# Kernel optimization log

Measured on AMD Instinct MI355X. Metric: run time of the kernel, lower is better.

## Reference

```python
import jax, jax.numpy as jnp
import numpy as np

B, T = 256, 1024
V, E, H = 27, 64, 128


def setup_inputs() -> dict:
    key = jax.random.key(0)
    ks = jax.random.split(key, 8)
    return {
        "x": jax.random.randint(ks[0], (B, T), 0, V, dtype=jnp.int32),
        "emb": jax.random.normal(ks[1], (V, E), dtype=jnp.float32) * 0.02,
        "wx0": jax.random.normal(ks[2], (E, 4 * H), dtype=jnp.float32) * 0.01,
        "wh0": jax.random.normal(ks[3], (H, 4 * H), dtype=jnp.float32) * 0.01,
        "b0": jnp.zeros((4 * H,), dtype=jnp.float32),
        "wx1": jax.random.normal(ks[4], (H, 4 * H), dtype=jnp.float32) * 0.01,
        "wh1": jax.random.normal(ks[5], (H, 4 * H), dtype=jnp.float32) * 0.01,
        "b1": jnp.zeros((4 * H,), dtype=jnp.float32),
        "why": jax.random.normal(ks[6], (H, V), dtype=jnp.float32),
        "by": jnp.zeros((V,), dtype=jnp.float32),
    }


def _cell(xt, h_prev, c_prev, wx, wh, b):
    # gates: [B, 4H]; chunk order matches torch .chunk(4): f, i, g, o
    gates = xt @ wx + h_prev @ wh + b
    ft, it, gt, ot = jnp.split(gates, 4, axis=1)
    c_t = jax.nn.sigmoid(ft) * c_prev + jax.nn.sigmoid(it) * jnp.tanh(gt)
    h_t = jnp.tanh(c_t) * jax.nn.sigmoid(ot)
    return h_t, c_t


def reference(x, emb, wx0, wh0, b0, wx1, wh1, b1, why, by):
    Bx = x.shape[0]
    xe = emb[x]                       # [B, T, E]
    xe = jnp.swapaxes(xe, 0, 1)       # [T, B, E] for scan over time
    h0 = jnp.zeros((Bx, H), jnp.float32)
    c0 = jnp.zeros((Bx, H), jnp.float32)
    h1 = jnp.zeros((Bx, H), jnp.float32)
    c1 = jnp.zeros((Bx, H), jnp.float32)

    def step(carry, xt):
        h0, c0, h1, c1 = carry
        h0, c0 = _cell(xt, h0, c0, wx0, wh0, b0)   # layer 0
        h1, c1 = _cell(h0, h1, c1, wx1, wh1, b1)   # layer 1 (dropout off in eval)
        yt = h1 @ why + by                         # [B, V]
        return (h0, c0, h1, c1), yt

    _, ys = jax.lax.scan(step, (h0, c0, h1, c1), xe)  # ys: [T, B, V]
    return jnp.swapaxes(ys, 0, 1)                     # [B, T, V]
```

## Files before the change

kernel.cpp:

```cpp
#include <hip/hip_runtime.h>


#define B_  256
#define T_  1024
#define V_  27
#define E_  64
#define H_  128
#define G4  512
#define TPITCH 528

template <int CTRL>
__device__ __forceinline__ float dppmov(float v) {
    return __int_as_float(__builtin_amdgcn_update_dpp(
               0, __float_as_int(v), CTRL, 0xF, 0xF, true));
}
__device__ __forceinline__ float sum8(float v) {
    v += dppmov<0xB1>(v);
    v += dppmov<0x4E>(v);
    v += dppmov<0x141>(v);
    return v;
}
__device__ __forceinline__ float tanh_fast(float y) {
    const float t = __expf(2.f * y);
    return fmaf(-2.f, __builtin_amdgcn_rcpf(t + 1.f), 1.f);
}

#define REPEAT16(M) M(0) M(1) M(2) M(3) M(4) M(5) M(6) M(7) \
                    M(8) M(9) M(10) M(11) M(12) M(13) M(14) M(15)

#define DECLW(K) float wf##K, wi##K, wg##K, wo##K;
#define LOADW(K) wf##K = wrow[(size_t)(K)*G4 + p]; \
                 wi##K = wrow[(size_t)(K)*G4 + H_ + p]; \
                 wg##K = wrow[(size_t)(K)*G4 + 2*H_ + p]; \
                 wo##K = wrow[(size_t)(K)*G4 + 3*H_ + p];
#define FMAK(K, HV, C) sf = fmaf(HV.C, wf##K, sf); \
                       si = fmaf(HV.C, wi##K, si); \
                       sg_ = fmaf(HV.C, wg##K, sg_); \
                       so = fmaf(HV.C, wo##K, so);

__global__ __launch_bounds__(G4)
void build_table0(const float* __restrict__ emb,
                  const float* __restrict__ wx0,
                  const float* __restrict__ b0,
                  float* __restrict__ table0)
{
    const int v = blockIdx.x;
    const int j = threadIdx.x;
    __shared__ float e[E_];
    if (j < E_) e[j] = emb[v * E_ + j];
    __syncthreads();
    float s = b0[j];
#pragma unroll 8
    for (int k = 0; k < E_; ++k) s += e[k] * wx0[k * G4 + j];
    const int r = j & (H_ - 1), gate = j >> 7;
    table0[v * TPITCH + gate * 132 + r] = s;
}

__global__ __launch_bounds__(1024, 4)
void lstm_l0_chunk(const int* __restrict__ x,
                   const float* __restrict__ table0,
                   const float* __restrict__ wh0,
                   float* __restrict__ h0st, float* __restrict__ c0st,
                   float* __restrict__ h0buf,
                   int t0, int TC)
{
    const int j = threadIdx.x;
    const int p = j >> 3;
    const int e = j & 7;
    const int b = blockIdx.x;
    const int gate = e & 3;

    __shared__ __align__(16) float hP[2][8][20];

    const float* wrow = wh0 + (size_t)(16 * e) * G4;
    REPEAT16(DECLW)
    REPEAT16(LOADW)
    if (j < H_) hP[0][j >> 4][j & 15] = h0st[b * H_ + j];
    float c = c0st[b * H_ + p];
    float hh = 0.f;
    __syncthreads();

    const int* xb = x + (size_t)b * T_ + t0;
    float* hob = h0buf + (size_t)b * TC * H_;
    const float A = (gate == 2) ? 2.f : 1.f;
    const int toff = gate * 132 + p;
    const bool e0 = (e & 1), e1 = (e & 2);

    float tv = table0[xb[0] * TPITCH + toff];
    for (int t = 0; t < TC; ++t) {
        const int idxn = (t + 1 < TC) ? xb[t + 1] : 0;

        const float4* hb4 = reinterpret_cast<const float4*>(&hP[t & 1][e][0]);
        const float4 h0v = hb4[0], h1v = hb4[1], h2v = hb4[2], h3v = hb4[3];

        float sf = 0.f, si = 0.f, sg_ = 0.f, so = 0.f;
        FMAK(0,  h0v, x) FMAK(1,  h0v, y) FMAK(2,  h0v, z) FMAK(3,  h0v, w)
        FMAK(4,  h1v, x) FMAK(5,  h1v, y) FMAK(6,  h1v, z) FMAK(7,  h1v, w)
        FMAK(8,  h2v, x) FMAK(9,  h2v, y) FMAK(10, h2v, z) FMAK(11, h2v, w)
        FMAK(12, h3v, x) FMAK(13, h3v, y) FMAK(14, h3v, z) FMAK(15, h3v, w)

        const float rf = sum8(sf);
        const float ri = sum8(si);
        const float rg = sum8(sg_);
        const float ro = sum8(so);

        const float s0 = e0 ? ri : rf;
        const float s1 = e0 ? ro : rg;
        const float val = (e1 ? s1 : s0) + tv;

        const float tz  = __expf(A * val);
        const float act = fmaf(-A, __builtin_amdgcn_rcpf(tz + 1.f), 1.f);

        const float iv = dppmov<0x39>(act);
        const float gv = dppmov<0x4E>(act);
        const float ov = dppmov<0x93>(act);
        c  = fmaf(act, c, iv * gv);
        hh = tanh_fast(c) * ov;

        if (e == 0) {
            hP[(t + 1) & 1][p >> 4][p & 15] = hh;
            hob[(size_t)t * H_ + p] = hh;
        }
        tv = table0[idxn * TPITCH + toff];
        __syncthreads();
    }
    if (e == 0) { h0st[b * H_ + p] = hh; c0st[b * H_ + p] = c; }
}

__global__ __launch_bounds__(G4, 2)
void gemm_xg1(const float* __restrict__ h0buf,
              const float* __restrict__ wx1,
              const float* __restrict__ b1,
              float* __restrict__ xg1)
{
    const int j  = threadIdx.x;
    const size_t m0 = (size_t)blockIdx.x * 64;
    const int c  = j & 127;
    const int rg = j >> 7;

    __shared__ __align__(16) float aT[64 * 132];

#pragma unroll
    for (int i = 0; i < 4; ++i) {
        const int e  = i * G4 + j;
        const int r  = e >> 5;
        const int k4 = e & 31;
        const float4 v = *reinterpret_cast<const float4*>(&h0buf[(m0 + r) * H_ + k4 * 4]);
        *reinterpret_cast<float4*>(&aT[r * 132 + k4 * 4]) = v;
    }
    __syncthreads();

    float acc[4][16];
#pragma unroll
    for (int cc = 0; cc < 4; ++cc)
#pragma unroll
        for (int rr = 0; rr < 16; ++rr) acc[cc][rr] = 0.f;

    for (int k4 = 0; k4 < 32; ++k4) {
        float bv[4][4];
#pragma unroll
        for (int kk = 0; kk < 4; ++kk)
#pragma unroll
            for (int cc = 0; cc < 4; ++cc)
                bv[kk][cc] = wx1[(size_t)(k4 * 4 + kk) * G4 + cc * 128 + c];
#pragma unroll
        for (int rr = 0; rr < 16; ++rr) {
            const float4 av = *reinterpret_cast<const float4*>(&aT[(rg * 16 + rr) * 132 + k4 * 4]);
#pragma unroll
            for (int cc = 0; cc < 4; ++cc) {
                acc[cc][rr] = fmaf(av.x, bv[0][cc], acc[cc][rr]);
                acc[cc][rr] = fmaf(av.y, bv[1][cc], acc[cc][rr]);
                acc[cc][rr] = fmaf(av.z, bv[2][cc], acc[cc][rr]);
                acc[cc][rr] = fmaf(av.w, bv[3][cc], acc[cc][rr]);
            }
        }
    }

    float b1v[4];
#pragma unroll
    for (int cc = 0; cc < 4; ++cc) b1v[cc] = b1[cc * 128 + c];
#pragma unroll
    for (int rr = 0; rr < 16; ++rr) {
        const size_t row = m0 + rg * 16 + rr;
#pragma unroll
        for (int cc = 0; cc < 4; ++cc)
            xg1[row * G4 + cc * 128 + c] = acc[cc][rr] + b1v[cc];
    }
}

__global__ __launch_bounds__(1024, 4)
void lstm_l1_chunk(const float* __restrict__ xg1,
                   const float* __restrict__ wh1,
                   float* __restrict__ h1st, float* __restrict__ c1st,
                   float* __restrict__ h1buf,
                   int TC)
{
    const int j = threadIdx.x;
    const int p = j >> 3;
    const int e = j & 7;
    const int b = blockIdx.x;
    const int gate = e & 3;

    __shared__ __align__(16) float hP[2][8][20];

    const float* wrow = wh1 + (size_t)(16 * e) * G4;
    REPEAT16(DECLW)
    REPEAT16(LOADW)
    if (j < H_) hP[0][j >> 4][j & 15] = h1st[b * H_ + j];
    float c = c1st[b * H_ + p];
    float hh = 0.f;
    __syncthreads();

    const float* xgb = xg1 + (size_t)b * TC * G4;
    float* hob = h1buf + (size_t)b * TC * H_;
    const float A = (gate == 2) ? 2.f : 1.f;
    const int xcol = gate * H_ + p;
    const bool e0 = (e & 1), e1 = (e & 2);

    float xv = xgb[xcol];
    for (int t = 0; t < TC; ++t) {
        const float xvn = (t + 1 < TC) ? xgb[(size_t)(t + 1) * G4 + xcol] : 0.f;

        const float4* hb4 = reinterpret_cast<const float4*>(&hP[t & 1][e][0]);
        const float4 h0v = hb4[0], h1v = hb4[1], h2v = hb4[2], h3v = hb4[3];

        float sf = 0.f, si = 0.f, sg_ = 0.f, so = 0.f;
        FMAK(0,  h0v, x) FMAK(1,  h0v, y) FMAK(2,  h0v, z) FMAK(3,  h0v, w)
        FMAK(4,  h1v, x) FMAK(5,  h1v, y) FMAK(6,  h1v, z) FMAK(7,  h1v, w)
        FMAK(8,  h2v, x) FMAK(9,  h2v, y) FMAK(10, h2v, z) FMAK(11, h2v, w)
        FMAK(12, h3v, x) FMAK(13, h3v, y) FMAK(14, h3v, z) FMAK(15, h3v, w)

        const float rf = sum8(sf);
        const float ri = sum8(si);
        const float rg = sum8(sg_);
        const float ro = sum8(so);

        const float s0 = e0 ? ri : rf;
        const float s1 = e0 ? ro : rg;
        const float val = (e1 ? s1 : s0) + xv;

        const float tz  = __expf(A * val);
        const float act = fmaf(-A, __builtin_amdgcn_rcpf(tz + 1.f), 1.f);

        const float iv = dppmov<0x39>(act);
        const float gv = dppmov<0x4E>(act);
        const float ov = dppmov<0x93>(act);
        c  = fmaf(act, c, iv * gv);
        hh = tanh_fast(c) * ov;

        if (e == 0) {
            hP[(t + 1) & 1][p >> 4][p & 15] = hh;
            hob[(size_t)t * H_ + p] = hh;
        }
        xv = xvn;
        __syncthreads();
    }
    if (e == 0) { h1st[b * H_ + p] = hh; c1st[b * H_ + p] = c; }
}

__global__ __launch_bounds__(256)
void proj_y(const float* __restrict__ h1buf,
            const float* __restrict__ why,
            const float* __restrict__ by,
            float* __restrict__ out,
            int t0, int TC)
{
    const int tid = threadIdx.x;
    const int b   = blockIdx.x;

    __shared__ __align__(16) float whyS[V_][H_];
    __shared__ float byS[V_];
    __shared__ float yS[256][29];

    for (int e = tid; e < V_ * H_; e += 256) {
        const int v = e / H_, k = e - v * H_;
        whyS[v][k] = why[k * V_ + v];
    }
    if (tid < V_) byS[tid] = by[tid];
    __syncthreads();

    const float* hb  = h1buf + (size_t)b * TC * H_;
    float* outb      = out + ((size_t)b * T_ + t0) * V_;

    for (int tt0 = 0; tt0 < TC; tt0 += 256) {
        const int tt = tt0 + tid;
        if (tt < TC) {
            float acc[V_];
#pragma unroll
            for (int v = 0; v < V_; ++v) acc[v] = byS[v];
            const float4* hr = reinterpret_cast<const float4*>(hb + (size_t)tt * H_);
#pragma unroll 4
            for (int k4 = 0; k4 < 32; ++k4) {
                const float4 hv = hr[k4];
#pragma unroll
                for (int v = 0; v < V_; ++v) {
                    const float4 wv = *reinterpret_cast<const float4*>(&whyS[v][k4 * 4]);
                    acc[v] = fmaf(hv.x, wv.x,
                             fmaf(hv.y, wv.y,
                             fmaf(hv.z, wv.z,
                             fmaf(hv.w, wv.w, acc[v]))));
                }
            }
#pragma unroll
            for (int v = 0; v < V_; ++v) yS[tid][v] = acc[v];
        }
        __syncthreads();
        const int nrow = (TC - tt0 < 256) ? (TC - tt0) : 256;
        const int n = nrow * V_;
        float* od = outb + (size_t)tt0 * V_;
        for (int i = tid; i < n; i += 256) {
            const int r = i / V_, v = i - r * V_;
            od[i] = yS[r][v];
        }
        __syncthreads();
    }
}

__global__ __launch_bounds__(G4, 1)
void lstm_persist(const int* __restrict__ x,
                  const float* __restrict__ table0,
                  const float* __restrict__ wh0,
                  const float* __restrict__ wx1,
                  const float* __restrict__ wh1,
                  const float* __restrict__ b1,
                  const float* __restrict__ why,
                  const float* __restrict__ by,
                  float* __restrict__ out)
{
    const int j  = threadIdx.x;
    const int bb = blockIdx.x * 2;

    __shared__ float h0s[2][H_], c0s[2][H_], h1s[2][H_], c1s[2][H_];
    __shared__ float hcat[2][2 * H_];
    __shared__ float g0s[2][G4], g1s[2][G4];
    __shared__ float whyS[H_ * V_];
    __shared__ float b1S[G4];
    __shared__ float byS[V_];
    __shared__ float pb[2][V_][8];

    for (int i = j; i < H_ * V_; i += G4) whyS[i] = why[i];
    b1S[j] = b1[j];
    if (j < V_) byS[j] = by[j];
    if (j < H_) {
        h0s[0][j] = 0.f; h0s[1][j] = 0.f; c0s[0][j] = 0.f; c0s[1][j] = 0.f;
        h1s[0][j] = 0.f; h1s[1][j] = 0.f; c1s[0][j] = 0.f; c1s[1][j] = 0.f;
    }
    __syncthreads();

    const int* xA = x + (size_t)(bb + 0) * T_;
    const int* xB = x + (size_t)(bb + 1) * T_;
    float* outA = out + (size_t)(bb + 0) * T_ * V_;
    float* outB = out + (size_t)(bb + 1) * T_ * V_;

    const int tix = (j >> 7) * 132 + (j & (H_ - 1));

    for (int t = 0; t < T_; ++t) {
        const int ia = xA[t];
        const int ib = xB[t];
        float aA = table0[ia * TPITCH + tix];
        float aB = table0[ib * TPITCH + tix];
#pragma unroll 8
        for (int k = 0; k < H_; ++k) {
            const float w = wh0[k * G4 + j];
            aA += h0s[0][k] * w;
            aB += h0s[1][k] * w;
        }
        g0s[0][j] = aA; g0s[1][j] = aB;
        __syncthreads();

        if (j < 2 * H_) {
            const int gi = j >> 7, r = j & (H_ - 1);
            const float f  = 1.f / (1.f + expf(-g0s[gi][r]));
            const float i_ = 1.f / (1.f + expf(-g0s[gi][H_ + r]));
            const float g  = tanhf(g0s[gi][2 * H_ + r]);
            const float o  = 1.f / (1.f + expf(-g0s[gi][3 * H_ + r]));
            const float c  = f * c0s[gi][r] + i_ * g;
            c0s[gi][r] = c;
            const float h = tanhf(c) * o;
            h0s[gi][r] = h;
            hcat[gi][r] = h;
            hcat[gi][H_ + r] = h1s[gi][r];
        }
        __syncthreads();

        float bA = b1S[j];
        float bB = bA;
#pragma unroll 8
        for (int k = 0; k < H_; ++k) {
            const float w = wx1[k * G4 + j];
            bA += hcat[0][k] * w;
            bB += hcat[1][k] * w;
        }
#pragma unroll 8
        for (int k = 0; k < H_; ++k) {
            const float w = wh1[k * G4 + j];
            bA += hcat[0][H_ + k] * w;
            bB += hcat[1][H_ + k] * w;
        }
        g1s[0][j] = bA; g1s[1][j] = bB;
        __syncthreads();

        if (j < 2 * H_) {
            const int gi = j >> 7, r = j & (H_ - 1);
            const float f  = 1.f / (1.f + expf(-g1s[gi][r]));
            const float i_ = 1.f / (1.f + expf(-g1s[gi][H_ + r]));
            const float g  = tanhf(g1s[gi][2 * H_ + r]);
            const float o  = 1.f / (1.f + expf(-g1s[gi][3 * H_ + r]));
            const float c  = f * c1s[gi][r] + i_ * g;
            c1s[gi][r] = c;
            h1s[gi][r] = tanhf(c) * o;
        }
        __syncthreads();

        if (j < 2 * V_ * 8) {
            int qq = j;
            const int gi = (qq >= V_ * 8) ? 1 : 0;
            qq -= gi * V_ * 8;
            const int v = qq >> 3, kk = qq & 7;
            float pv = 0.f;
#pragma unroll
            for (int k = kk * 16; k < kk * 16 + 16; ++k)
                pv += h1s[gi][k] * whyS[k * V_ + v];
            pb[gi][v][kk] = pv;
        }
        __syncthreads();

        if (j < 2 * V_) {
            const int gi = (j >= V_) ? 1 : 0;
            const int v  = j - gi * V_;
            float s = byS[v];
#pragma unroll
            for (int qq = 0; qq < 8; ++qq) s += pb[gi][v][qq];
            (gi ? outB : outA)[t * V_ + v] = s;
        }
        __syncthreads();
    }
}

extern "C" void kernel_launch(void* const* d_in, const int* in_sizes, int n_in,
                              void* d_out, int out_size, void* d_ws, size_t ws_size,
                              hipStream_t stream)
{
    const int*   x   = (const int*)  d_in[0];
    const float* emb = (const float*)d_in[1];
    const float* wx0 = (const float*)d_in[2];
    const float* wh0 = (const float*)d_in[3];
    const float* b0  = (const float*)d_in[4];
    const float* wx1 = (const float*)d_in[5];
    const float* wh1 = (const float*)d_in[6];
    const float* b1  = (const float*)d_in[7];
    const float* why = (const float*)d_in[8];
    const float* by  = (const float*)d_in[9];
    float* out = (float*)d_out;
    float* wsf = (float*)d_ws;

    const size_t tabF   = (size_t)V_ * TPITCH;
    const size_t stateF = (size_t)4 * B_ * H_;

    int TC = 0;
    for (int tc = T_; tc >= 32; tc >>= 1) {
        const size_t need = (tabF + stateF + (size_t)B_ * tc * (H_ + G4 + H_)) * 4;
        if (need <= ws_size) { TC = tc; break; }
    }

    float* table0 = wsf;
    build_table0<<<dim3(V_), dim3(G4), 0, stream>>>(emb, wx0, b0, table0);

    if (TC == 0) {
        lstm_persist<<<dim3(B_ / 2), dim3(G4), 0, stream>>>(
            x, table0, wh0, wx1, wh1, b1, why, by, out);
        return;
    }

    float* h0st   = wsf + tabF;
    float* c0st   = h0st + (size_t)B_ * H_;
    float* h1st   = c0st + (size_t)B_ * H_;
    float* c1st   = h1st + (size_t)B_ * H_;
    float* h0buf  = c1st + (size_t)B_ * H_;
    float* xg1buf = h0buf + (size_t)B_ * TC * H_;
    float* h1buf  = xg1buf + (size_t)B_ * TC * G4;

    (void)hipMemsetAsync(h0st, 0, stateF * sizeof(float), stream);

    const int NC = T_ / TC;
    for (int c = 0; c < NC; ++c) {
        const int t0 = c * TC;
        lstm_l0_chunk<<<dim3(B_), dim3(1024), 0, stream>>>(
            x, table0, wh0, h0st, c0st, h0buf, t0, TC);
        gemm_xg1<<<dim3(4 * TC), dim3(G4), 0, stream>>>(
            h0buf, wx1, b1, xg1buf);
        lstm_l1_chunk<<<dim3(B_), dim3(1024), 0, stream>>>(
            xg1buf, wh1, h1st, c1st, h1buf, TC);
        proj_y<<<dim3(B_), dim3(256), 0, stream>>>(
            h1buf, why, by, out, t0, TC);
    }
}
```

Before: 2.087 ms.

## Halve LSTM recurrent block size by computing two hidden units per thread

Both recurrent LSTM kernels drop from 1024 to 512 threads per block. Each thread now keeps weights for two adjacent hidden units across all four gates over its 16-row k-slice (128 register weights) and accumulates eight partial sums. After the cross-lane reductions, a three-level select picks each lane's gate and unit. The aim is to cut per-step barrier and wave-scheduling overhead with fewer waves per block, at the cost of twice the register pressure and longer per-thread FMA chains, leaving fewer waves to hide latency.

```diff
diff --git a/kernel.cpp b/kernel.cpp
--- a/kernel.cpp
+++ b/kernel.cpp
@@ -28,15 +28,17 @@
 #define REPEAT16(M) M(0) M(1) M(2) M(3) M(4) M(5) M(6) M(7) \
                     M(8) M(9) M(10) M(11) M(12) M(13) M(14) M(15)
 
-#define DECLW(K) float wf##K, wi##K, wg##K, wo##K;
-#define LOADW(K) wf##K = wrow[(size_t)(K)*G4 + p]; \
-                 wi##K = wrow[(size_t)(K)*G4 + H_ + p]; \
-                 wg##K = wrow[(size_t)(K)*G4 + 2*H_ + p]; \
-                 wo##K = wrow[(size_t)(K)*G4 + 3*H_ + p];
-#define FMAK(K, HV, C) sf = fmaf(HV.C, wf##K, sf); \
-                       si = fmaf(HV.C, wi##K, si); \
-                       sg_ = fmaf(HV.C, wg##K, sg_); \
-                       so = fmaf(HV.C, wo##K, so);
+#define DECLW(K) float w0_##K, w1_##K, w2_##K, w3_##K, w4_##K, w5_##K, w6_##K, w7_##K;
+#define LOADW(K) { const float* r0 = wmat + (size_t)(16 * s + (K)) * G4 + 2 * o; \
+                   w0_##K = r0[0];          w1_##K = r0[H_]; \
+                   w2_##K = r0[2 * H_];     w3_##K = r0[3 * H_]; \
+                   w4_##K = r0[1];          w5_##K = r0[H_ + 1]; \
+                   w6_##K = r0[2 * H_ + 1]; w7_##K = r0[3 * H_ + 1]; }
+#define FMAK(K, HVAL) { const float hv_ = (HVAL); \
+    a0 = fmaf(hv_, w0_##K, a0); a1 = fmaf(hv_, w1_##K, a1); \
+    a2 = fmaf(hv_, w2_##K, a2); a3 = fmaf(hv_, w3_##K, a3); \
+    a4 = fmaf(hv_, w4_##K, a4); a5 = fmaf(hv_, w5_##K, a5); \
+    a6 = fmaf(hv_, w6_##K, a6); a7 = fmaf(hv_, w7_##K, a7); }
 
 __global__ __launch_bounds__(G4)
 void build_table0(const float* __restrict__ emb,
@@ -49,14 +51,14 @@
     __shared__ float e[E_];
     if (j < E_) e[j] = emb[v * E_ + j];
     __syncthreads();
-    float s = b0[j];
+    float sacc = b0[j];
 #pragma unroll 8
-    for (int k = 0; k < E_; ++k) s += e[k] * wx0[k * G4 + j];
+    for (int k = 0; k < E_; ++k) sacc = fmaf(e[k], wx0[k * G4 + j], sacc);
     const int r = j & (H_ - 1), gate = j >> 7;
-    table0[v * TPITCH + gate * 132 + r] = s;
-}
-
-__global__ __launch_bounds__(1024, 4)
+    table0[v * TPITCH + gate * 132 + r] = sacc;
+}
+
+__global__ __launch_bounds__(512, 2)
 void lstm_l0_chunk(const int* __restrict__ x,
                    const float* __restrict__ table0,
                    const float* __restrict__ wh0,
@@ -65,48 +67,52 @@
                    int t0, int TC)
 {
     const int j = threadIdx.x;
-    const int p = j >> 3;
-    const int e = j & 7;
+    const int o = j >> 3;
+    const int s = j & 7;
     const int b = blockIdx.x;
-    const int gate = e & 3;
-
-    __shared__ __align__(16) float hP[2][8][20];
-
-    const float* wrow = wh0 + (size_t)(16 * e) * G4;
+    const int gl = s & 3;
+    const int rowL = 2 * o + (s >> 2);
+
+    __shared__ __align__(16) float hP[2][8][36];
+
+    const float* wmat = wh0;
     REPEAT16(DECLW)
     REPEAT16(LOADW)
     if (j < H_) hP[0][j >> 4][j & 15] = h0st[b * H_ + j];
-    float c = c0st[b * H_ + p];
+    float c = c0st[b * H_ + rowL];
     float hh = 0.f;
     __syncthreads();
 
     const int* xb = x + (size_t)b * T_ + t0;
     float* hob = h0buf + (size_t)b * TC * H_;
-    const float A = (gate == 2) ? 2.f : 1.f;
-    const int toff = gate * 132 + p;
-    const bool e0 = (e & 1), e1 = (e & 2);
+    const float A = (gl == 2) ? 2.f : 1.f;
+    const int toff = gl * 132 + rowL;
+    const bool s0 = (s & 1), s1 = (s & 2), s2 = (s & 4);
 
     float tv = table0[xb[0] * TPITCH + toff];
     for (int t = 0; t < TC; ++t) {
         const int idxn = (t + 1 < TC) ? xb[t + 1] : 0;
 
-        const float4* hb4 = reinterpret_cast<const float4*>(&hP[t & 1][e][0]);
-        const float4 h0v = hb4[0], h1v = hb4[1], h2v = hb4[2], h3v = hb4[3];
-
-        float sf = 0.f, si = 0.f, sg_ = 0.f, so = 0.f;
-        FMAK(0,  h0v, x) FMAK(1,  h0v, y) FMAK(2,  h0v, z) FMAK(3,  h0v, w)
-        FMAK(4,  h1v, x) FMAK(5,  h1v, y) FMAK(6,  h1v, z) FMAK(7,  h1v, w)
-        FMAK(8,  h2v, x) FMAK(9,  h2v, y) FMAK(10, h2v, z) FMAK(11, h2v, w)
-        FMAK(12, h3v, x) FMAK(13, h3v, y) FMAK(14, h3v, z) FMAK(15, h3v, w)
-
-        const float rf = sum8(sf);
-        const float ri = sum8(si);
-        const float rg = sum8(sg_);
-        const float ro = sum8(so);
-
-        const float s0 = e0 ? ri : rf;
-        const float s1 = e0 ? ro : rg;
-        const float val = (e1 ? s1 : s0) + tv;
+        const float4* hb4 = reinterpret_cast<const float4*>(&hP[t & 1][s][0]);
+        const float4 u0 = hb4[0], u1 = hb4[1], u2 = hb4[2], u3 = hb4[3];
+
+        float a0 = 0.f, a1 = 0.f, a2 = 0.f, a3 = 0.f,
+              a4 = 0.f, a5 = 0.f, a6 = 0.f, a7 = 0.f;
+        FMAK(0,  u0.x) FMAK(1,  u0.y) FMAK(2,  u0.z) FMAK(3,  u0.w)
+        FMAK(4,  u1.x) FMAK(5,  u1.y) FMAK(6,  u1.z) FMAK(7,  u1.w)
+        FMAK(8,  u2.x) FMAK(9,  u2.y) FMAK(10, u2.z) FMAK(11, u2.w)
+        FMAK(12, u3.x) FMAK(13, u3.y) FMAK(14, u3.z) FMAK(15, u3.w)
+
+        a0 = sum8(a0); a1 = sum8(a1); a2 = sum8(a2); a3 = sum8(a3);
+        a4 = sum8(a4); a5 = sum8(a5); a6 = sum8(a6); a7 = sum8(a7);
+
+        const float t0_ = s0 ? a1 : a0;
+        const float t1_ = s0 ? a3 : a2;
+        const float t2_ = s0 ? a5 : a4;
+        const float t3_ = s0 ? a7 : a6;
+        const float u0_ = s1 ? t1_ : t0_;
+        const float u1_ = s1 ? t3_ : t2_;
+        const float val = (s2 ? u1_ : u0_) + tv;
 
         const float tz  = __expf(A * val);
         const float act = fmaf(-A, __builtin_amdgcn_rcpf(tz + 1.f), 1.f);
@@ -117,14 +123,14 @@
         c  = fmaf(act, c, iv * gv);
         hh = tanh_fast(c) * ov;
 
-        if (e == 0) {
-            hP[(t + 1) & 1][p >> 4][p & 15] = hh;
-            hob[(size_t)t * H_ + p] = hh;
+        if (gl == 0) {
+            hP[(t + 1) & 1][rowL >> 4][rowL & 15] = hh;
+            hob[(size_t)t * H_ + rowL] = hh;
         }
         tv = table0[idxn * TPITCH + toff];
         __syncthreads();
     }
-    if (e == 0) { h0st[b * H_ + p] = hh; c0st[b * H_ + p] = c; }
+    if (gl == 0) { h0st[b * H_ + rowL] = hh; c0st[b * H_ + rowL] = c; }
 }
 
 __global__ __launch_bounds__(G4, 2)
@@ -188,7 +194,7 @@
     }
 }
 
-__global__ __launch_bounds__(1024, 4)
+__global__ __launch_bounds__(512, 2)
 void lstm_l1_chunk(const float* __restrict__ xg1,
                    const float* __restrict__ wh1,
                    float* __restrict__ h1st, float* __restrict__ c1st,
@@ -196,48 +202,52 @@
                    int TC)
 {
     const int j = threadIdx.x;
-    const int p = j >> 3;
-    const int e = j & 7;
+    const int o = j >> 3;
+    const int s = j & 7;
     const int b = blockIdx.x;
-    const int gate = e & 3;
-
-    __shared__ __align__(16) float hP[2][8][20];
-
-    const float* wrow = wh1 + (size_t)(16 * e) * G4;
+    const int gl = s & 3;
+    const int rowL = 2 * o + (s >> 2);
+
+    __shared__ __align__(16) float hP[2][8][36];
+
+    const float* wmat = wh1;
     REPEAT16(DECLW)
     REPEAT16(LOADW)
     if (j < H_) hP[0][j >> 4][j & 15] = h1st[b * H_ + j];
-    float c = c1st[b * H_ + p];
+    float c = c1st[b * H_ + rowL];
     float hh = 0.f;
     __syncthreads();
 
     const float* xgb = xg1 + (size_t)b * TC * G4;
     float* hob = h1buf + (size_t)b * TC * H_;
-    const float A = (gate == 2) ? 2.f : 1.f;
-    const int xcol = gate * H_ + p;
-    const bool e0 = (e & 1), e1 = (e & 2);
+    const float A = (gl == 2) ? 2.f : 1.f;
+    const int xcol = gl * H_ + rowL;
+    const bool s0 = (s & 1), s1 = (s & 2), s2 = (s & 4);
 
     float xv = xgb[xcol];
     for (int t = 0; t < TC; ++t) {
         const float xvn = (t + 1 < TC) ? xgb[(size_t)(t + 1) * G4 + xcol] : 0.f;
 
-        const float4* hb4 = reinterpret_cast<const float4*>(&hP[t & 1][e][0]);
-        const float4 h0v = hb4[0], h1v = hb4[1], h2v = hb4[2], h3v = hb4[3];
-
-        float sf = 0.f, si = 0.f, sg_ = 0.f, so = 0.f;
-        FMAK(0,  h0v, x) FMAK(1,  h0v, y) FMAK(2,  h0v, z) FMAK(3,  h0v, w)
-        FMAK(4,  h1v, x) FMAK(5,  h1v, y) FMAK(6,  h1v, z) FMAK(7,  h1v, w)
-        FMAK(8,  h2v, x) FMAK(9,  h2v, y) FMAK(10, h2v, z) FMAK(11, h2v, w)
-        FMAK(12, h3v, x) FMAK(13, h3v, y) FMAK(14, h3v, z) FMAK(15, h3v, w)
-
-        const float rf = sum8(sf);
-        const float ri = sum8(si);
-        const float rg = sum8(sg_);
-        const float ro = sum8(so);
-
-        const float s0 = e0 ? ri : rf;
-        const float s1 = e0 ? ro : rg;
-        const float val = (e1 ? s1 : s0) + xv;
+        const float4* hb4 = reinterpret_cast<const float4*>(&hP[t & 1][s][0]);
+        const float4 u0 = hb4[0], u1 = hb4[1], u2 = hb4[2], u3 = hb4[3];
+
+        float a0 = 0.f, a1 = 0.f, a2 = 0.f, a3 = 0.f,
+              a4 = 0.f, a5 = 0.f, a6 = 0.f, a7 = 0.f;
+        FMAK(0,  u0.x) FMAK(1,  u0.y) FMAK(2,  u0.z) FMAK(3,  u0.w)
+        FMAK(4,  u1.x) FMAK(5,  u1.y) FMAK(6,  u1.z) FMAK(7,  u1.w)
+        FMAK(8,  u2.x) FMAK(9,  u2.y) FMAK(10, u2.z) FMAK(11, u2.w)
+        FMAK(12, u3.x) FMAK(13, u3.y) FMAK(14, u3.z) FMAK(15, u3.w)
+
+        a0 = sum8(a0); a1 = sum8(a1); a2 = sum8(a2); a3 = sum8(a3);
+        a4 = sum8(a4); a5 = sum8(a5); a6 = sum8(a6); a7 = sum8(a7);
+
+        const float t0_ = s0 ? a1 : a0;
+        const float t1_ = s0 ? a3 : a2;
+        const float t2_ = s0 ? a5 : a4;
+        const float t3_ = s0 ? a7 : a6;
+        const float u0_ = s1 ? t1_ : t0_;
+        const float u1_ = s1 ? t3_ : t2_;
+        const float val = (s2 ? u1_ : u0_) + xv;
 
         const float tz  = __expf(A * val);
         const float act = fmaf(-A, __builtin_amdgcn_rcpf(tz + 1.f), 1.f);
@@ -248,14 +258,14 @@
         c  = fmaf(act, c, iv * gv);
         hh = tanh_fast(c) * ov;
 
-        if (e == 0) {
-            hP[(t + 1) & 1][p >> 4][p & 15] = hh;
-            hob[(size_t)t * H_ + p] = hh;
+        if (gl == 0) {
+            hP[(t + 1) & 1][rowL >> 4][rowL & 15] = hh;
+            hob[(size_t)t * H_ + rowL] = hh;
         }
         xv = xvn;
         __syncthreads();
     }
-    if (e == 0) { h1st[b * H_ + p] = hh; c1st[b * H_ + p] = c; }
+    if (gl == 0) { h1st[b * H_ + rowL] = hh; c1st[b * H_ + rowL] = c; }
 }
 
 __global__ __launch_bounds__(256)
@@ -428,10 +438,10 @@
         if (j < 2 * V_) {
             const int gi = (j >= V_) ? 1 : 0;
             const int v  = j - gi * V_;
-            float s = byS[v];
-#pragma unroll
-            for (int qq = 0; qq < 8; ++qq) s += pb[gi][v][qq];
-            (gi ? outB : outA)[t * V_ + v] = s;
+            float sA = byS[v];
+#pragma unroll
+            for (int qq = 0; qq < 8; ++qq) sA += pb[gi][v][qq];
+            (gi ? outB : outA)[t * V_ + v] = sA;
         }
         __syncthreads();
     }
@@ -485,11 +495,11 @@
     const int NC = T_ / TC;
     for (int c = 0; c < NC; ++c) {
         const int t0 = c * TC;
-        lstm_l0_chunk<<<dim3(B_), dim3(1024), 0, stream>>>(
+        lstm_l0_chunk<<<dim3(B_), dim3(512), 0, stream>>>(
             x, table0, wh0, h0st, c0st, h0buf, t0, TC);
         gemm_xg1<<<dim3(4 * TC), dim3(G4), 0, stream>>>(
             h0buf, wx1, b1, xg1buf);
-        lstm_l1_chunk<<<dim3(B_), dim3(1024), 0, stream>>>(
+        lstm_l1_chunk<<<dim3(B_), dim3(512), 0, stream>>>(
             xg1buf, wh1, h1st, c1st, h1buf, TC);
         proj_y<<<dim3(B_), dim3(256), 0, stream>>>(
             h1buf, why, by, out, t0, TC);
```

New measurement: 2.000 ms. 4.2% less time.
